# Kernel optimization log

Measured on AMD Instinct MI355X. Metric: run time of the kernel, lower is better.

Reference implementation:

```python
import jax, jax.numpy as jnp
import numpy as np

N, H, DH = 8, 12, 64          # batch, heads, head dim (embedding_dim=768)
LV, LA = 1568, 512            # video / audio token counts
NCV, NCA = 392, 256           # candidates kept: LV*(1-0.75), LA*(1-0.5)
SCALE = DH ** -0.5            # avmatching_module.scale


def setup_inputs() -> dict:
    key = jax.random.key(0)
    ks = jax.random.split(key, 14)
    f32 = jnp.float32
    return {
        "pos_v_q": jax.random.normal(ks[0], (N, H, LV, DH), f32),
        "pos_v_k": jax.random.normal(ks[1], (N, H, LV, DH), f32),
        "pos_a_q": jax.random.normal(ks[2], (N, H, LA, DH), f32),
        "pos_a_k": jax.random.normal(ks[3], (N, H, LA, DH), f32),
        "pos_cross_att_av": jax.random.uniform(ks[4], (N, H, LA, LV), f32),
        "pos_cross_att_va": jax.random.uniform(ks[5], (N, H, LV, LA), f32),
        "n_attn_av": jax.random.uniform(ks[6], (N, LV), f32, 0.01, 1.0),
        "n_attn_va": jax.random.uniform(ks[7], (N, LA), f32, 0.01, 1.0),
        "spu_a_cls": jax.random.normal(ks[8], (N, H, DH), f32),
        "spu_v_cls": jax.random.normal(ks[9], (N, H, DH), f32),
        "u_v": jax.random.uniform(ks[10], (N, LV), f32),
        "u_a": jax.random.uniform(ks[11], (N, LA), f32),
        # att ids come from argsort of attention scores in the original -> permutations
        "att_av_ids": jnp.argsort(jax.random.uniform(ks[12], (N, LV)), axis=1),
        "att_va_ids": jnp.argsort(jax.random.uniform(ks[13], (N, LA)), axis=1),
    }


def _pipeline(pos_v_q, pos_v_k, pos_a_q, pos_a_k, pos_cross_att_av, pos_cross_att_va,
              n_attn_av, n_attn_va, spu_a_cls, spu_v_cls, u_v, u_a,
              att_av_ids, att_va_ids):
    idx_v = att_av_ids[:, :NCV]   # kept video token ids
    idx_a = att_va_ids[:, :NCA]   # kept audio token ids

    # --- gather kept tokens (torch.gather dim=2) and attention-weighted cls pooling ---
    d_v_k = jnp.take_along_axis(pos_v_k, idx_v[:, None, :, None], axis=2)   # [N,H,NCV,DH]
    v_tok = jnp.take_along_axis(pos_v_q, idx_v[:, None, :, None], axis=2)
    d_n_av = jnp.take_along_axis(n_attn_av, idx_v, axis=1)                  # [N,NCV]
    pos_v_cls = jnp.einsum('nhld,nl->nhd', v_tok, d_n_av) / jnp.sum(d_n_av, 1)[:, None, None]

    d_a_k = jnp.take_along_axis(pos_a_k, idx_a[:, None, :, None], axis=2)   # [N,H,NCA,DH]
    a_tok = jnp.take_along_axis(pos_a_q, idx_a[:, None, :, None], axis=2)
    d_n_va = jnp.take_along_axis(n_attn_va, idx_a, axis=1)                  # [N,NCA]
    pos_a_cls = jnp.einsum('nhld,nl->nhd', a_tok, d_n_va) / jnp.sum(d_n_va, 1)[:, None, None]

    # --- video keep probability: spurious (buffer audio query) vs positive attention ---
    v_spu = jnp.einsum('nhld,nhd->nhl', d_v_k, spu_a_cls) * SCALE           # [N,H,NCV]
    v_pos = jnp.take_along_axis(pos_cross_att_av, idx_v[:, None, None, :], axis=3)  # [N,H,LA,NCV]
    v_pos = jnp.take_along_axis(v_pos, idx_a[:, None, :, None], axis=2)     # [N,H,NCA,NCV]
    v_pos = jnp.einsum('nhal,na->nhl', v_pos, d_n_va) / jnp.sum(d_n_va, 1)[:, None, None]
    v_att = jax.nn.softmax(jnp.stack([v_spu, v_pos], axis=-1), axis=-1).mean(axis=1)
    prob_v = v_att[..., 0]                                                  # [N,NCV]
    restore_v = jnp.argsort(att_av_ids, axis=1)
    prob_v_full = jnp.take_along_axis(
        jnp.concatenate([prob_v, jnp.zeros((prob_v.shape[0], LV - NCV), prob_v.dtype)], axis=1),
        restore_v, axis=1)                                                  # [N,LV]

    # --- audio keep probability: spurious (buffer video query) vs positive attention ---
    a_spu = jnp.einsum('nhld,nhd->nhl', d_a_k, spu_v_cls) * SCALE           # [N,H,NCA]
    a_pos = jnp.take_along_axis(pos_cross_att_va, idx_a[:, None, None, :], axis=3)  # [N,H,LV,NCA]
    a_pos = jnp.take_along_axis(a_pos, idx_v[:, None, :, None], axis=2)     # [N,H,NCV,NCA]
    a_pos = jnp.einsum('nhvl,nv->nhl', a_pos, d_n_av) / jnp.sum(d_n_av, 1)[:, None, None]
    a_att = jax.nn.softmax(jnp.stack([a_spu, a_pos], axis=-1), axis=-1).mean(axis=1)
    prob_a = a_att[..., 0]                                                  # [N,NCA]
    restore_a = jnp.argsort(att_va_ids, axis=1)
    prob_a_full = jnp.take_along_axis(
        jnp.concatenate([prob_a, jnp.zeros((prob_a.shape[0], LA - NCA), prob_a.dtype)], axis=1),
        restore_a, axis=1)                                                  # [N,LA]

    # --- bernoulli pruning, deterministic via external uniforms (u < p == bernoulli(p)) ---
    prune_n_av = jnp.where(u_v < prob_v_full, 0.0, n_attn_av)
    prune_n_va = jnp.where(u_a < prob_a_full, 0.0, n_attn_va)

    n = prob_v_full.shape[0]
    return jnp.concatenate([prob_v_full, prob_a_full,
                            pos_v_cls.reshape(n, -1), pos_a_cls.reshape(n, -1),
                            prune_n_av, prune_n_va], axis=1)


def reference(pos_v_q, pos_v_k, pos_a_q, pos_a_k, pos_cross_att_av, pos_cross_att_va,
              n_attn_av, n_attn_va, spu_a_cls, spu_v_cls, u_v, u_a,
              att_av_ids, att_va_ids):
    return _pipeline(pos_v_q, pos_v_k, pos_a_q, pos_a_k, pos_cross_att_av,
                     pos_cross_att_va, n_attn_av, n_attn_va, spu_a_cls, spu_v_cls,
                     u_v, u_a, att_av_ids, att_va_ids)
```

## Files before the change

kernel.cpp:

```cpp
#include <hip/hip_runtime.h>

#define NN 8
#define HH 12
#define DH 64
#define LV 1568
#define LA 512
#define NCV 392
#define NCA 256
#define SCALE 0.125f

#define OUT_STRIDE (LV + LA + 2 * HH * DH + LV + LA)
#define OFF_PROB_V 0
#define OFF_PROB_A (LV)
#define OFF_VCLS   (LV + LA)
#define OFF_ACLS   (LV + LA + HH * DH)
#define OFF_PR_AV  (LV + LA + 2 * HH * DH)
#define OFF_PR_VA  (LV + LA + 2 * HH * DH + LV)

#define CHA 8
#define CHV 8

#define WS_RV      0
#define WS_RA      (CHA * NN * HH * LV)
#define WS_INV_SAV (WS_RA + CHV * NN * HH * LA)
#define WS_INV_SVA (WS_INV_SAV + NN)

#define B_INV   NN
#define B_CLS   (2 * NN * HH)
#define B_RAV   (NN * HH * CHA)
#define B_RVA   (NN * HH * CHV)
#define GRID_S1 (B_INV + B_CLS + B_RAV + B_RVA)

__global__ __launch_bounds__(256) void stage1_kernel(
        const float* __restrict__ pvq,
        const float* __restrict__ paq,
        const float* __restrict__ av,
        const float* __restrict__ va,
        const int* __restrict__ av_ids,
        const int* __restrict__ va_ids,
        const float* __restrict__ n_av,
        const float* __restrict__ n_va,
        float* __restrict__ ws,
        float* __restrict__ out) {
    int b = blockIdx.x;
    int t = threadIdx.x;
    __shared__ float red[4][DH];
    __shared__ float wred[4];
    __shared__ int   sIdx[64];
    __shared__ float sW[64];

    if (b < B_INV) {
        int n = b;
        float vs = 0.f, as = 0.f;
        for (int l = t; l < NCV; l += 256) vs += n_av[n * LV + av_ids[n * LV + l]];
        if (t < NCA) as = n_va[n * LA + va_ids[n * LA + t]];
        for (int m = 32; m; m >>= 1) { vs += __shfl_xor(vs, m); as += __shfl_xor(as, m); }
        int wave = t >> 6;
        if ((t & 63) == 0) { red[wave][0] = vs; wred[wave] = as; }
        __syncthreads();
        if (t == 0) {
            float S0 = red[0][0] + red[1][0] + red[2][0] + red[3][0];
            float S1 = wred[0] + wred[1] + wred[2] + wred[3];
            ws[WS_INV_SAV + n] = 1.f / S0;
            ws[WS_INV_SVA + n] = 1.f / S1;
        }
        return;
    }
    b -= B_INV;

    if (b < B_CLS) {
        int wave = t >> 6, lane = t & 63;
        if (b < NN * HH) {
            int n = b / HH, h = b % HH;
            float acc = 0.f, wsum = 0.f;
            for (int l = wave; l < NCV; l += 4) {
                int ridx = av_ids[n * LV + l];
                float w  = n_av[n * LV + ridx];
                acc  += pvq[((size_t)b * LV + ridx) * DH + lane] * w;
                wsum += w;
            }
            red[wave][lane] = acc;
            if (lane == 0) wred[wave] = wsum;
            __syncthreads();
            if (wave == 0) {
                float s = red[0][lane] + red[1][lane] + red[2][lane] + red[3][lane];
                float W = wred[0] + wred[1] + wred[2] + wred[3];
                out[(size_t)n * OUT_STRIDE + OFF_VCLS + h * DH + lane] = s / W;
            }
        } else {
            int b2 = b - NN * HH;
            int n = b2 / HH, h = b2 % HH;
            float acc = 0.f, wsum = 0.f;
            for (int l = wave; l < NCA; l += 4) {
                int ridx = va_ids[n * LA + l];
                float w  = n_va[n * LA + ridx];
                acc  += paq[((size_t)b2 * LA + ridx) * DH + lane] * w;
                wsum += w;
            }
            red[wave][lane] = acc;
            if (lane == 0) wred[wave] = wsum;
            __syncthreads();
            if (wave == 0) {
                float s = red[0][lane] + red[1][lane] + red[2][lane] + red[3][lane];
                float W = wred[0] + wred[1] + wred[2] + wred[3];
                out[(size_t)n * OUT_STRIDE + OFF_ACLS + h * DH + lane] = s / W;
            }
        }
        return;
    }
    b -= B_CLS;

    if (b < B_RAV) {
        int chunk = b % CHA;
        int nh    = b / CHA;
        int n     = nh / HH;
        const int rows = NCA / CHA;
        if (t < rows) {
            int ridx = va_ids[n * LA + chunk * rows + t];
            sIdx[t] = ridx;
            sW[t]   = n_va[n * LA + ridx];
        }
        __syncthreads();
        float4 acc0 = {0.f, 0.f, 0.f, 0.f};
        float4 acc1 = {0.f, 0.f, 0.f, 0.f};
        const int c0 = t;
        const int c1 = t + 256;
        const bool has1 = (c1 < LV / 4);
        #pragma unroll 4
        for (int r = 0; r < rows; ++r) {
            float w = sW[r];
            const float4* row = (const float4*)(av + ((size_t)nh * LA + sIdx[r]) * LV);
            float4 x0 = row[c0];
            acc0.x += x0.x * w; acc0.y += x0.y * w; acc0.z += x0.z * w; acc0.w += x0.w * w;
            if (has1) {
                float4 x1 = row[c1];
                acc1.x += x1.x * w; acc1.y += x1.y * w; acc1.z += x1.z * w; acc1.w += x1.w * w;
            }
        }
        float4* outp = (float4*)(ws + WS_RV + ((size_t)chunk * NN * HH + nh) * LV);
        outp[c0] = acc0;
        if (has1) outp[c1] = acc1;
        return;
    }
    b -= B_RAV;

    {
        int chunk = b % CHV;
        int nh    = b / CHV;
        int n     = nh / HH;
        const int rows = NCV / CHV;
        if (t < rows) {
            int ridx = av_ids[n * LV + chunk * rows + t];
            sIdx[t] = ridx;
            sW[t]   = n_av[n * LV + ridx];
        }
        __syncthreads();
        float2 acc = {0.f, 0.f};
        #pragma unroll 4
        for (int r = 0; r < rows; ++r) {
            float w = sW[r];
            const float2* row = (const float2*)(va + ((size_t)nh * LV + sIdx[r]) * LA);
            float2 x = row[t];
            acc.x += x.x * w; acc.y += x.y * w;
        }
        ((float2*)(ws + WS_RA + ((size_t)chunk * NN * HH + nh) * LA))[t] = acc;
    }
}

#define MAIN_W  (NN * NCV + NN * NCA)
#define MAIN_B  (MAIN_W / 4)
#define TAILV   (NN * (LV - NCV))
#define TAILA   (NN * (LA - NCA))
#define TAIL_B  ((TAILV + TAILA + 255) / 256)
#define GRID_PB (MAIN_B + TAIL_B)

__global__ __launch_bounds__(256) void prob_kernel(
        const float* __restrict__ pvk,
        const float* __restrict__ pak,
        const float* __restrict__ spu_a,
        const float* __restrict__ spu_v,
        const int* __restrict__ av_ids,
        const int* __restrict__ va_ids,
        const float* __restrict__ n_av,
        const float* __restrict__ n_va,
        const float* __restrict__ u_v,
        const float* __restrict__ u_a,
        const float* __restrict__ ws,
        float* __restrict__ out) {
    if (blockIdx.x < MAIN_B) {
        int W = blockIdx.x * 4 + (threadIdx.x >> 6);
        int lane = threadIdx.x & 63;
        if (W < NN * NCV) {
            int n = W / NCV, l = W % NCV;
            int col = av_ids[n * LV + l];
            float invS = ws[WS_INV_SVA + n];
            float psum = 0.f;
            #pragma unroll
            for (int h = 0; h < HH; ++h) {
                int nh = n * HH + h;
                float prod = pvk[((size_t)nh * LV + col) * DH + lane] * spu_a[nh * DH + lane];
                for (int m = 32; m; m >>= 1) prod += __shfl_xor(prod, m);
                float pos = 0.f;
                #pragma unroll
                for (int p = 0; p < CHA; ++p)
                    pos += ws[WS_RV + ((size_t)p * NN * HH + nh) * LV + col];
                psum += 1.f / (1.f + __expf(pos * invS - prod * SCALE));
            }
            float pm = psum * (1.f / HH);
            if (lane == 0) {
                out[(size_t)n * OUT_STRIDE + OFF_PROB_V + col] = pm;
                float uv = u_v[n * LV + col];
                out[(size_t)n * OUT_STRIDE + OFF_PR_AV + col] =
                    (uv < pm) ? 0.f : n_av[n * LV + col];
            }
        } else {
            int W2 = W - NN * NCV;
            int n = W2 / NCA, l = W2 % NCA;
            int col = va_ids[n * LA + l];
            float invS = ws[WS_INV_SAV + n];
            float psum = 0.f;
            #pragma unroll
            for (int h = 0; h < HH; ++h) {
                int nh = n * HH + h;
                float prod = pak[((size_t)nh * LA + col) * DH + lane] * spu_v[nh * DH + lane];
                for (int m = 32; m; m >>= 1) prod += __shfl_xor(prod, m);
                float pos = 0.f;
                #pragma unroll
                for (int p = 0; p < CHV; ++p)
                    pos += ws[WS_RA + ((size_t)p * NN * HH + nh) * LA + col];
                psum += 1.f / (1.f + __expf(pos * invS - prod * SCALE));
            }
            float pm = psum * (1.f / HH);
            if (lane == 0) {
                out[(size_t)n * OUT_STRIDE + OFF_PROB_A + col] = pm;
                float ua = u_a[n * LA + col];
                out[(size_t)n * OUT_STRIDE + OFF_PR_VA + col] =
                    (ua < pm) ? 0.f : n_va[n * LA + col];
            }
        }
    } else {
        int tid = (blockIdx.x - MAIN_B) * 256 + threadIdx.x;
        if (tid < TAILV) {
            int n = tid / (LV - NCV), l = NCV + tid % (LV - NCV);
            int col = av_ids[n * LV + l];
            out[(size_t)n * OUT_STRIDE + OFF_PROB_V + col] = 0.f;
            out[(size_t)n * OUT_STRIDE + OFF_PR_AV + col] = n_av[n * LV + col];
        } else if (tid < TAILV + TAILA) {
            int i = tid - TAILV;
            int n = i / (LA - NCA), l = NCA + i % (LA - NCA);
            int col = va_ids[n * LA + l];
            out[(size_t)n * OUT_STRIDE + OFF_PROB_A + col] = 0.f;
            out[(size_t)n * OUT_STRIDE + OFF_PR_VA + col] = n_va[n * LA + col];
        }
    }
}

extern "C" void kernel_launch(void* const* d_in, const int* in_sizes, int n_in,
                              void* d_out, int out_size, void* d_ws, size_t ws_size,
                              hipStream_t stream) {
    const float* pvq   = (const float*)d_in[0];
    const float* pvk   = (const float*)d_in[1];
    const float* paq   = (const float*)d_in[2];
    const float* pak   = (const float*)d_in[3];
    const float* av    = (const float*)d_in[4];
    const float* va    = (const float*)d_in[5];
    const float* n_av  = (const float*)d_in[6];
    const float* n_va  = (const float*)d_in[7];
    const float* spu_a = (const float*)d_in[8];
    const float* spu_v = (const float*)d_in[9];
    const float* u_v   = (const float*)d_in[10];
    const float* u_a   = (const float*)d_in[11];
    const int* av_ids  = (const int*)d_in[12];
    const int* va_ids  = (const int*)d_in[13];
    float* out = (float*)d_out;
    float* ws  = (float*)d_ws;

    stage1_kernel<<<GRID_S1, 256, 0, stream>>>(pvq, paq, av, va, av_ids, va_ids,
                                               n_av, n_va, ws, out);
    prob_kernel<<<GRID_PB, 256, 0, stream>>>(pvk, pak, spu_a, spu_v,
                                             av_ids, va_ids, n_av, n_va,
                                             u_v, u_a, ws, out);
}
```

Baseline: 628.4 us.

## Move spu dot products and tail scatter into stage1, slim prob kernel

```diff
diff --git a/kernel.cpp b/kernel.cpp
--- a/kernel.cpp
+++ b/kernel.cpp
@@ -8,6 +8,7 @@
 #define NCV 392
 #define NCA 256
 #define SCALE 0.125f
+#define NTOK (NCV + NCA)
 
 #define OUT_STRIDE (LV + LA + 2 * HH * DH + LV + LA)
 #define OFF_PROB_V 0
@@ -17,25 +18,33 @@
 #define OFF_PR_AV  (LV + LA + 2 * HH * DH)
 #define OFF_PR_VA  (LV + LA + 2 * HH * DH + LV)
 
-#define CHA 8
-#define CHV 8
+#define CH 4
 
 #define WS_RV      0
-#define WS_RA      (CHA * NN * HH * LV)
-#define WS_INV_SAV (WS_RA + CHV * NN * HH * LA)
+#define WS_RA      (CH * NN * HH * LV)
+#define WS_SPU     (WS_RA + CH * NN * HH * LA)
+#define WS_INV_SAV (WS_SPU + NN * NTOK * HH)
 #define WS_INV_SVA (WS_INV_SAV + NN)
 
+#define B_RAV   (NN * HH * CH)
+#define B_RVA   (NN * HH * CH)
+#define B_SPU   (NN * NTOK / 4)
+#define B_CLS   (2 * NN * HH)
 #define B_INV   NN
-#define B_CLS   (2 * NN * HH)
-#define B_RAV   (NN * HH * CHA)
-#define B_RVA   (NN * HH * CHV)
-#define GRID_S1 (B_INV + B_CLS + B_RAV + B_RVA)
+#define TAILV   (NN * (LV - NCV))
+#define TAILA   (NN * (LA - NCA))
+#define B_TAIL  ((TAILV + TAILA + 255) / 256)
+#define GRID_S1 (B_RAV + B_RVA + B_SPU + B_CLS + B_INV + B_TAIL)
 
 __global__ __launch_bounds__(256) void stage1_kernel(
         const float* __restrict__ pvq,
         const float* __restrict__ paq,
+        const float* __restrict__ pvk,
+        const float* __restrict__ pak,
         const float* __restrict__ av,
         const float* __restrict__ va,
+        const float* __restrict__ spu_a,
+        const float* __restrict__ spu_v,
         const int* __restrict__ av_ids,
         const int* __restrict__ va_ids,
         const float* __restrict__ n_av,
@@ -46,79 +55,18 @@
     int t = threadIdx.x;
     __shared__ float red[4][DH];
     __shared__ float wred[4];
-    __shared__ int   sIdx[64];
-    __shared__ float sW[64];
-
-    if (b < B_INV) {
-        int n = b;
-        float vs = 0.f, as = 0.f;
-        for (int l = t; l < NCV; l += 256) vs += n_av[n * LV + av_ids[n * LV + l]];
-        if (t < NCA) as = n_va[n * LA + va_ids[n * LA + t]];
-        for (int m = 32; m; m >>= 1) { vs += __shfl_xor(vs, m); as += __shfl_xor(as, m); }
-        int wave = t >> 6;
-        if ((t & 63) == 0) { red[wave][0] = vs; wred[wave] = as; }
-        __syncthreads();
-        if (t == 0) {
-            float S0 = red[0][0] + red[1][0] + red[2][0] + red[3][0];
-            float S1 = wred[0] + wred[1] + wred[2] + wred[3];
-            ws[WS_INV_SAV + n] = 1.f / S0;
-            ws[WS_INV_SVA + n] = 1.f / S1;
-        }
-        return;
-    }
-    b -= B_INV;
-
-    if (b < B_CLS) {
-        int wave = t >> 6, lane = t & 63;
-        if (b < NN * HH) {
-            int n = b / HH, h = b % HH;
-            float acc = 0.f, wsum = 0.f;
-            for (int l = wave; l < NCV; l += 4) {
-                int ridx = av_ids[n * LV + l];
-                float w  = n_av[n * LV + ridx];
-                acc  += pvq[((size_t)b * LV + ridx) * DH + lane] * w;
-                wsum += w;
-            }
-            red[wave][lane] = acc;
-            if (lane == 0) wred[wave] = wsum;
-            __syncthreads();
-            if (wave == 0) {
-                float s = red[0][lane] + red[1][lane] + red[2][lane] + red[3][lane];
-                float W = wred[0] + wred[1] + wred[2] + wred[3];
-                out[(size_t)n * OUT_STRIDE + OFF_VCLS + h * DH + lane] = s / W;
-            }
-        } else {
-            int b2 = b - NN * HH;
-            int n = b2 / HH, h = b2 % HH;
-            float acc = 0.f, wsum = 0.f;
-            for (int l = wave; l < NCA; l += 4) {
-                int ridx = va_ids[n * LA + l];
-                float w  = n_va[n * LA + ridx];
-                acc  += paq[((size_t)b2 * LA + ridx) * DH + lane] * w;
-                wsum += w;
-            }
-            red[wave][lane] = acc;
-            if (lane == 0) wred[wave] = wsum;
-            __syncthreads();
-            if (wave == 0) {
-                float s = red[0][lane] + red[1][lane] + red[2][lane] + red[3][lane];
-                float W = wred[0] + wred[1] + wred[2] + wred[3];
-                out[(size_t)n * OUT_STRIDE + OFF_ACLS + h * DH + lane] = s / W;
-            }
-        }
-        return;
-    }
-    b -= B_CLS;
+    __shared__ int   sIdx[128];
+    __shared__ float sW[128];
 
     if (b < B_RAV) {
-        int chunk = b % CHA;
-        int nh    = b / CHA;
+        int chunk = b % CH;
+        int nh    = b / CH;
         int n     = nh / HH;
-        const int rows = NCA / CHA;
-        if (t < rows) {
-            int ridx = va_ids[n * LA + chunk * rows + t];
-            sIdx[t] = ridx;
-            sW[t]   = n_va[n * LA + ridx];
+        const int rows = NCA / CH;
+        for (int r = t; r < rows; r += 256) {
+            int ridx = va_ids[n * LA + chunk * rows + r];
+            sIdx[r] = ridx;
+            sW[r]   = n_va[n * LA + ridx];
         }
         __syncthreads();
         float4 acc0 = {0.f, 0.f, 0.f, 0.f};
@@ -144,15 +92,15 @@
     }
     b -= B_RAV;
 
-    {
-        int chunk = b % CHV;
-        int nh    = b / CHV;
+    if (b < B_RVA) {
+        int chunk = b % CH;
+        int nh    = b / CH;
         int n     = nh / HH;
-        const int rows = NCV / CHV;
-        if (t < rows) {
-            int ridx = av_ids[n * LV + chunk * rows + t];
-            sIdx[t] = ridx;
-            sW[t]   = n_av[n * LV + ridx];
+        const int rows = NCV / CH;
+        for (int r = t; r < rows; r += 256) {
+            int ridx = av_ids[n * LV + chunk * rows + r];
+            sIdx[r] = ridx;
+            sW[r]   = n_av[n * LV + ridx];
         }
         __syncthreads();
         float2 acc = {0.f, 0.f};
@@ -164,82 +112,101 @@
             acc.x += x.x * w; acc.y += x.y * w;
         }
         ((float2*)(ws + WS_RA + ((size_t)chunk * NN * HH + nh) * LA))[t] = acc;
-    }
-}
-
-#define MAIN_W  (NN * NCV + NN * NCA)
-#define MAIN_B  (MAIN_W / 4)
-#define TAILV   (NN * (LV - NCV))
-#define TAILA   (NN * (LA - NCA))
-#define TAIL_B  ((TAILV + TAILA + 255) / 256)
-#define GRID_PB (MAIN_B + TAIL_B)
-
-__global__ __launch_bounds__(256) void prob_kernel(
-        const float* __restrict__ pvk,
-        const float* __restrict__ pak,
-        const float* __restrict__ spu_a,
-        const float* __restrict__ spu_v,
-        const int* __restrict__ av_ids,
-        const int* __restrict__ va_ids,
-        const float* __restrict__ n_av,
-        const float* __restrict__ n_va,
-        const float* __restrict__ u_v,
-        const float* __restrict__ u_a,
-        const float* __restrict__ ws,
-        float* __restrict__ out) {
-    if (blockIdx.x < MAIN_B) {
-        int W = blockIdx.x * 4 + (threadIdx.x >> 6);
-        int lane = threadIdx.x & 63;
-        if (W < NN * NCV) {
-            int n = W / NCV, l = W % NCV;
-            int col = av_ids[n * LV + l];
-            float invS = ws[WS_INV_SVA + n];
-            float psum = 0.f;
+        return;
+    }
+    b -= B_RVA;
+
+    if (b < B_SPU) {
+        int W = b * 4 + (t >> 6);
+        int lane = t & 63;
+        int n = W / NTOK, lc = W % NTOK;
+        if (lc < NCV) {
+            int col = av_ids[n * LV + lc];
             #pragma unroll
             for (int h = 0; h < HH; ++h) {
                 int nh = n * HH + h;
                 float prod = pvk[((size_t)nh * LV + col) * DH + lane] * spu_a[nh * DH + lane];
                 for (int m = 32; m; m >>= 1) prod += __shfl_xor(prod, m);
-                float pos = 0.f;
-                #pragma unroll
-                for (int p = 0; p < CHA; ++p)
-                    pos += ws[WS_RV + ((size_t)p * NN * HH + nh) * LV + col];
-                psum += 1.f / (1.f + __expf(pos * invS - prod * SCALE));
-            }
-            float pm = psum * (1.f / HH);
-            if (lane == 0) {
-                out[(size_t)n * OUT_STRIDE + OFF_PROB_V + col] = pm;
-                float uv = u_v[n * LV + col];
-                out[(size_t)n * OUT_STRIDE + OFF_PR_AV + col] =
-                    (uv < pm) ? 0.f : n_av[n * LV + col];
+                if (lane == 0) ws[WS_SPU + (size_t)W * HH + h] = prod * SCALE;
             }
         } else {
-            int W2 = W - NN * NCV;
-            int n = W2 / NCA, l = W2 % NCA;
+            int l = lc - NCV;
             int col = va_ids[n * LA + l];
-            float invS = ws[WS_INV_SAV + n];
-            float psum = 0.f;
             #pragma unroll
             for (int h = 0; h < HH; ++h) {
                 int nh = n * HH + h;
                 float prod = pak[((size_t)nh * LA + col) * DH + lane] * spu_v[nh * DH + lane];
                 for (int m = 32; m; m >>= 1) prod += __shfl_xor(prod, m);
-                float pos = 0.f;
-                #pragma unroll
-                for (int p = 0; p < CHV; ++p)
-                    pos += ws[WS_RA + ((size_t)p * NN * HH + nh) * LA + col];
-                psum += 1.f / (1.f + __expf(pos * invS - prod * SCALE));
-            }
-            float pm = psum * (1.f / HH);
-            if (lane == 0) {
-                out[(size_t)n * OUT_STRIDE + OFF_PROB_A + col] = pm;
-                float ua = u_a[n * LA + col];
-                out[(size_t)n * OUT_STRIDE + OFF_PR_VA + col] =
-                    (ua < pm) ? 0.f : n_va[n * LA + col];
-            }
-        }
-    } else {
-        int tid = (blockIdx.x - MAIN_B) * 256 + threadIdx.x;
+                if (lane == 0) ws[WS_SPU + (size_t)W * HH + h] = prod * SCALE;
+            }
+        }
+        return;
+    }
+    b -= B_SPU;
+
+    if (b < B_CLS) {
+        int wave = t >> 6, lane = t & 63;
+        if (b < NN * HH) {
+            int n = b / HH, h = b % HH;
+            float acc = 0.f, wsum = 0.f;
+            for (int l = wave; l < NCV; l += 4) {
+                int ridx = av_ids[n * LV + l];
+                float w  = n_av[n * LV + ridx];
+                acc  += pvq[((size_t)b * LV + ridx) * DH + lane] * w;
+                wsum += w;
+            }
+            red[wave][lane] = acc;
+            if (lane == 0) wred[wave] = wsum;
+            __syncthreads();
+            if (wave == 0) {
+                float s = red[0][lane] + red[1][lane] + red[2][lane] + red[3][lane];
+                float W = wred[0] + wred[1] + wred[2] + wred[3];
+                out[(size_t)n * OUT_STRIDE + OFF_VCLS + h * DH + lane] = s / W;
+            }
+        } else {
+            int b2 = b - NN * HH;
+            int n = b2 / HH, h = b2 % HH;
+            float acc = 0.f, wsum = 0.f;
+            for (int l = wave; l < NCA; l += 4) {
+                int ridx = va_ids[n * LA + l];
+                float w  = n_va[n * LA + ridx];
+                acc  += paq[((size_t)b2 * LA + ridx) * DH + lane] * w;
+                wsum += w;
+            }
+            red[wave][lane] = acc;
+            if (lane == 0) wred[wave] = wsum;
+            __syncthreads();
+            if (wave == 0) {
+                float s = red[0][lane] + red[1][lane] + red[2][lane] + red[3][lane];
+                float W = wred[0] + wred[1] + wred[2] + wred[3];
+                out[(size_t)n * OUT_STRIDE + OFF_ACLS + h * DH + lane] = s / W;
+            }
+        }
+        return;
+    }
+    b -= B_CLS;
+
+    if (b < B_INV) {
+        int n = b;
+        float vs = 0.f, as = 0.f;
+        for (int l = t; l < NCV; l += 256) vs += n_av[n * LV + av_ids[n * LV + l]];
+        if (t < NCA) as = n_va[n * LA + va_ids[n * LA + t]];
+        for (int m = 32; m; m >>= 1) { vs += __shfl_xor(vs, m); as += __shfl_xor(as, m); }
+        int wave = t >> 6;
+        if ((t & 63) == 0) { red[wave][0] = vs; wred[wave] = as; }
+        __syncthreads();
+        if (t == 0) {
+            float S0 = red[0][0] + red[1][0] + red[2][0] + red[3][0];
+            float S1 = wred[0] + wred[1] + wred[2] + wred[3];
+            ws[WS_INV_SAV + n] = 1.f / S0;
+            ws[WS_INV_SVA + n] = 1.f / S1;
+        }
+        return;
+    }
+    b -= B_INV;
+
+    {
+        int tid = b * 256 + t;
         if (tid < TAILV) {
             int n = tid / (LV - NCV), l = NCV + tid % (LV - NCV);
             int col = av_ids[n * LV + l];
@@ -251,6 +218,65 @@
             int col = va_ids[n * LA + l];
             out[(size_t)n * OUT_STRIDE + OFF_PROB_A + col] = 0.f;
             out[(size_t)n * OUT_STRIDE + OFF_PR_VA + col] = n_va[n * LA + col];
+        }
+    }
+}
+
+#define GRID_PB (NN * NTOK / 4)
+
+__global__ __launch_bounds__(256) void prob2_kernel(
+        const int* __restrict__ av_ids,
+        const int* __restrict__ va_ids,
+        const float* __restrict__ n_av,
+        const float* __restrict__ n_va,
+        const float* __restrict__ u_v,
+        const float* __restrict__ u_a,
+        const float* __restrict__ ws,
+        float* __restrict__ out) {
+    int W = blockIdx.x * 4 + (threadIdx.x >> 6);
+    int lane = threadIdx.x & 63;
+    int n = W / NTOK, lc = W % NTOK;
+    bool isV = (lc < NCV);
+    int h = lane >> 2, p = lane & 3;
+
+    int col;
+    float invS, part = 0.f;
+    if (isV) {
+        col  = av_ids[n * LV + lc];
+        invS = ws[WS_INV_SVA + n];
+        if (lane < 48)
+            part = ws[WS_RV + ((size_t)p * NN * HH + n * HH + h) * LV + col];
+    } else {
+        col  = va_ids[n * LA + (lc - NCV)];
+        invS = ws[WS_INV_SAV + n];
+        if (lane < 48)
+            part = ws[WS_RA + ((size_t)p * NN * HH + n * HH + h) * LA + col];
+    }
+    part += __shfl_xor(part, 1);
+    part += __shfl_xor(part, 2);
+
+    float sig = 0.f;
+    if (lane < 48 && (lane & 3) == 0) {
+        float spu = ws[WS_SPU + (size_t)W * HH + h];
+        sig = 1.f / (1.f + __expf(part * invS - spu));
+    }
+    sig += __shfl_xor(sig, 4);
+    sig += __shfl_xor(sig, 8);
+    sig += __shfl_xor(sig, 16);
+    sig += __shfl_xor(sig, 32);
+
+    if (lane == 0) {
+        float pm = sig * (1.f / HH);
+        if (isV) {
+            out[(size_t)n * OUT_STRIDE + OFF_PROB_V + col] = pm;
+            float uv = u_v[n * LV + col];
+            out[(size_t)n * OUT_STRIDE + OFF_PR_AV + col] =
+                (uv < pm) ? 0.f : n_av[n * LV + col];
+        } else {
+            out[(size_t)n * OUT_STRIDE + OFF_PROB_A + col] = pm;
+            float ua = u_a[n * LA + col];
+            out[(size_t)n * OUT_STRIDE + OFF_PR_VA + col] =
+                (ua < pm) ? 0.f : n_va[n * LA + col];
         }
     }
 }
@@ -275,9 +301,9 @@
     float* out = (float*)d_out;
     float* ws  = (float*)d_ws;
 
-    stage1_kernel<<<GRID_S1, 256, 0, stream>>>(pvq, paq, av, va, av_ids, va_ids,
+    stage1_kernel<<<GRID_S1, 256, 0, stream>>>(pvq, paq, pvk, pak, av, va,
+                                               spu_a, spu_v, av_ids, va_ids,
                                                n_av, n_va, ws, out);
-    prob_kernel<<<GRID_PB, 256, 0, stream>>>(pvk, pak, spu_a, spu_v,
-                                             av_ids, va_ids, n_av, n_va,
-                                             u_v, u_a, ws, out);
+    prob2_kernel<<<GRID_PB, 256, 0, stream>>>(av_ids, va_ids, n_av, n_va,
+                                              u_v, u_a, ws, out);
 }
```

Measured after the change: 630.4 us. About the same (+0.3%).
